# Kernel optimization log

Measured on AMD Instinct MI355X. Metric: run time of the kernel, lower is better.

## Reference

```python
import jax, jax.numpy as jnp
import numpy as np

L, N, H, SQ = 24, 16384, 128, 32
D_OP, D_ATTR, D_FILT, D_OUT = 16, 56, 74, 32
D_IN = 2 * SQ + D_OP + D_ATTR  # 136
EPS = 1e-5
SLOPE = 0.01  # LeakyReLU default


def setup_inputs() -> dict:
    key = jax.random.key(0)
    ks = jax.random.split(key, 24)
    f32 = jnp.float32
    inp = {
        'op_pad': jax.random.normal(ks[0], (L, N, D_OP), f32),
        'attr_pad': jax.random.normal(ks[1], (L, N, D_ATTR), f32),
        'filter_pad': jax.random.normal(ks[2], (L, N, D_FILT), f32),
        'output_pad': jax.random.normal(ks[3], (L, N, D_OUT), f32),
        'mapping_pad': jax.random.randint(ks[4], (L, N, 2), 0, N + 1, jnp.int32),
        'batch_size': 4096,
        # filter / output squeeze linears
        'Wf': jax.random.normal(ks[5], (SQ, D_FILT), f32) * 0.05,
        'bf': jax.random.normal(ks[6], (SQ,), f32) * 0.05,
        'Wo': jax.random.normal(ks[7], (SQ, D_OUT), f32) * 0.05,
        'bo': jax.random.normal(ks[8], (SQ,), f32) * 0.05,
        # batchnorm affine params
        'g1': jnp.ones((SQ,), f32), 'beta1': jnp.zeros((SQ,), f32),
        'g2': jnp.ones((SQ,), f32), 'beta2': jnp.zeros((SQ,), f32),
        # LSTM (PyTorch layout: gates i,f,g,o stacked)
        'Wih': jax.random.normal(ks[9], (4 * H, D_IN), f32) * 0.05,
        'Whh': jax.random.normal(ks[10], (4 * H, H), f32) * 0.05,
        'bih': jax.random.normal(ks[11], (4 * H,), f32) * 0.05,
        'bhh': jax.random.normal(ks[12], (4 * H,), f32) * 0.05,
        # final MLP head
        'W1': jax.random.normal(ks[13], (20, H), f32) * 0.05,
        'b1': jax.random.normal(ks[14], (20,), f32) * 0.05,
        'W2': jax.random.normal(ks[15], (1, 20), f32) * 0.05,
        'b2': jax.random.normal(ks[16], (1,), f32) * 0.05,
    }
    return inp


def _leaky(x):
    return jnp.where(x > 0, x, SLOPE * x)


def _bn(x, g, b):
    # BatchNorm1d in training mode: batch stats (biased var), eps=1e-5
    m = jnp.mean(x, axis=0)
    v = jnp.var(x, axis=0)
    return (x - m) * jax.lax.rsqrt(v + EPS) * g + b


def _forward(op_pad, attr_pad, filter_pad, output_pad, mapping_pad, batch_size,
             Wf, bf, Wo, bo, g1, beta1, g2, beta2, Wih, Whh, bih, bhh, W1, b1, W2, b2):
    l, n = op_pad.shape[0], op_pad.shape[1]
    # squeeze filter / output features, flattened over (L*N)
    fd = _bn(_leaky(filter_pad.reshape(l * n, -1) @ Wf.T + bf), g1, beta1).reshape(l, n, SQ)
    od = _bn(_leaky(output_pad.reshape(l * n, -1) @ Wo.T + bo), g2, beta2).reshape(l, n, SQ)
    lstm_in = jnp.concatenate([op_pad, attr_pad, fd, od], axis=2)  # [L,N,D_IN]

    def step(carry, xs):
        h, c = carry                       # [N,H] previous level states
        x, mapping = xs                    # [N,D_IN], [N,2]
        mask = (mapping != 0)[..., None]   # [N,2,1]
        idx = jnp.maximum(mapping - 1, 0)  # [N,2] gather indices
        gh = jnp.sum(jnp.where(mask, h[idx], 0.0), axis=1) * 0.5  # [N,H]
        gc = jnp.sum(jnp.where(mask, c[idx], 0.0), axis=1) * 0.5
        gates = x @ Wih.T + bih + gh @ Whh.T + bhh  # [N,4H]
        i, f, g, o = jnp.split(gates, 4, axis=1)
        c_new = jax.nn.sigmoid(f) * gc + jax.nn.sigmoid(i) * jnp.tanh(g)
        h_new = jax.nn.sigmoid(o) * jnp.tanh(c_new)
        return (h_new, c_new), None

    z = jnp.zeros((n, H), lstm_in.dtype)
    # loop goes from the deepest level (index L-1) up to 0
    (h, _), _ = jax.lax.scan(step, (z, z), (lstm_in[::-1], mapping_pad[::-1]))
    out = h[:batch_size]
    out = jax.nn.sigmoid((out @ W1.T + b1) @ W2.T + b2)  # [B,1]
    return out


def reference(op_pad, attr_pad, filter_pad, output_pad, mapping_pad, batch_size,
              Wf, bf, Wo, bo, g1, beta1, g2, beta2, Wih, Whh, bih, bhh, W1, b1, W2, b2):
    return _forward(op_pad, attr_pad, filter_pad, output_pad, mapping_pad, batch_size,
                    Wf, bf, Wo, bo, g1, beta1, g2, beta2, Wih, Whh, bih, bhh, W1, b1, W2, b2)
```

## Files before the change

### kernel.cpp

```cpp
#include <hip/hip_runtime.h>
#include <hip/hip_bf16.h>

#define LL 24
#define NN 16384
#define HH 128
#define KP 288
#define LN (LL*NN)

typedef __bf16 bf16;
typedef __attribute__((ext_vector_type(8))) __bf16 bf16x8;
typedef __attribute__((ext_vector_type(2))) __bf16 bf16x2;
typedef __attribute__((ext_vector_type(4))) float f32x4;

__device__ __forceinline__ float sigm(float x){ return 1.f/(1.f+__expf(-x)); }
__device__ __forceinline__ float tanhfast(float x){
    float e = __expf(-2.f*fabsf(x));
    float t = (1.f-e)/(1.f+e);
    return x >= 0.f ? t : -t;
}
__device__ __forceinline__ void gld16(const void* g, void* l){
    __builtin_amdgcn_global_load_lds(
        (const __attribute__((address_space(1))) void*)g,
        (__attribute__((address_space(3))) void*)l, 16, 0, 0);
}

template<int D>
__global__ __launch_bounds__(256) void act_kernel(
    const float* __restrict__ X, const float* __restrict__ W,
    const float* __restrict__ bias, bf16* __restrict__ act,
    float* __restrict__ sums)
{
    __shared__ float w_lds[D*32];
    __shared__ float xs[128*D];
    const int tid = threadIdx.x;
    for (int i = tid; i < D*32; i += 256) {
        int k = i >> 5, ch = i & 31;
        w_lds[i] = W[ch*D + k];
    }
    const int c2 = tid & 15;
    const int rg = tid >> 4;
    const int ch0 = 2*c2, ch1 = ch0+1;
    const float b0 = bias[ch0], b1 = bias[ch1];
    float s0=0.f,s1=0.f,q0=0.f,q1=0.f;
    for (int tile = blockIdx.x; tile < LN/128; tile += gridDim.x) {
        const long row0 = (long)tile*128;
        __syncthreads();
        for (int i = tid; i < 128*D; i += 256) xs[i] = X[row0*D + i];
        __syncthreads();
        float a0[8], a1[8];
        #pragma unroll
        for (int i=0;i<8;++i){ a0[i]=b0; a1[i]=b1; }
        for (int k=0;k<D;++k){
            float w0 = w_lds[(k<<5)+ch0];
            float w1 = w_lds[(k<<5)+ch1];
            #pragma unroll
            for (int i=0;i<8;++i){
                float x = xs[(rg*8+i)*D + k];
                a0[i] = fmaf(x,w0,a0[i]);
                a1[i] = fmaf(x,w1,a1[i]);
            }
        }
        #pragma unroll
        for (int i=0;i<8;++i){
            float v0 = a0[i]; v0 = v0>0.f ? v0 : 0.01f*v0;
            float v1 = a1[i]; v1 = v1>0.f ? v1 : 0.01f*v1;
            bf16x2 pk; pk[0]=(bf16)v0; pk[1]=(bf16)v1;
            *(bf16x2*)&act[(row0 + rg*8+i)*32 + ch0] = pk;
            s0+=v0; q0+=v0*v0; s1+=v1; q1+=v1*v1;
        }
    }
    __syncthreads();
    float* red = xs;
    red[tid]=s0; red[256+tid]=q0; red[512+tid]=s1; red[768+tid]=q1;
    __syncthreads();
    if (tid < 16) {
        float ts0=0,tq0=0,ts1=0,tq1=0;
        for (int r=0;r<16;++r){
            int t = (r<<4) | tid;
            ts0+=red[t]; tq0+=red[256+t]; ts1+=red[512+t]; tq1+=red[768+t];
        }
        atomicAdd(&sums[2*tid],      ts0);
        atomicAdd(&sums[2*tid+1],    ts1);
        atomicAdd(&sums[32+2*tid],   tq0);
        atomicAdd(&sums[32+2*tid+1], tq1);
    }
}

__global__ void prep_wtb(const float* __restrict__ Wih, const float* __restrict__ Whh,
                         const float* __restrict__ bih, const float* __restrict__ bhh,
                         bf16* __restrict__ Wtb, float* __restrict__ b4p)
{
    const int np = blockIdx.x;
    const int k  = threadIdx.x;
    const int gate = (np>>4)&3;
    const int j = gate*128 + (np>>6)*16 + (np&15);
    if (k < KP) {
        float v = 0.f;
        if (k < 136)      v = Wih[(long)j*136 + k];
        else if (k >= 160) v = Whh[(long)j*128 + (k-160)];
        Wtb[(long)np*KP + k] = (bf16)v;
    }
    if (k == 0) b4p[np] = bih[j] + bhh[j];
}

__global__ void prep_stats(const float* __restrict__ stats,
    const float* __restrict__ g1, const float* __restrict__ beta1,
    const float* __restrict__ g2, const float* __restrict__ beta2,
    const float* __restrict__ W1, const float* __restrict__ b1,
    const float* __restrict__ W2, const float* __restrict__ b2,
    float* __restrict__ ss, float* __restrict__ wvb)
{
    const int t = threadIdx.x;
    const float inv = 1.f/(float)LN;
    if (t < 32) {
        float mean = stats[t]*inv;
        float var  = stats[32+t]*inv - mean*mean;
        float sc = g1[t]/sqrtf(var + 1e-5f);
        ss[t] = sc; ss[32+t] = beta1[t] - mean*sc;
    } else if (t < 64) {
        int c = t - 32;
        float mean = stats[64+c]*inv;
        float var  = stats[96+c]*inv - mean*mean;
        float sc = g2[c]/sqrtf(var + 1e-5f);
        ss[64+c] = sc; ss[96+c] = beta2[c] - mean*sc;
    }
    float s = 0.f;
    for (int a=0;a<20;++a) s += W2[a]*W1[a*HH + t];
    wvb[t] = s;
    if (t == 0) {
        float sb = 0.f;
        for (int a=0;a<20;++a) sb += W2[a]*b1[a];
        wvb[128] = sb + b2[0];
    }
}

__global__ __launch_bounds__(256) void build_a(
    const float* __restrict__ op, const float* __restrict__ attr,
    const bf16* __restrict__ actf, const bf16* __restrict__ acto,
    const int* __restrict__ map, const float* __restrict__ ss,
    const bf16* __restrict__ h_prev, bf16* __restrict__ A,
    int l, int first)
{
    const int n0 = blockIdx.x * 32;
    const long lbase = (long)l * NN;
    for (int i = threadIdx.x; i < 32*36; i += 256) {
        const int r = i / 36, c = i - r*36;
        const long n = n0 + r;
        const long e = lbase + n;
        const int k0 = c*8;
        bf16x8 out;
        if (c < 9) {
            const float* src = (c < 2) ? (op + e*16 + k0) : (attr + e*56 + (k0-16));
            float4 f0 = *(const float4*)src;
            float4 f1 = *(const float4*)(src+4);
            out[0]=(bf16)f0.x; out[1]=(bf16)f0.y; out[2]=(bf16)f0.z; out[3]=(bf16)f0.w;
            out[4]=(bf16)f1.x; out[5]=(bf16)f1.y; out[6]=(bf16)f1.z; out[7]=(bf16)f1.w;
        } else if (c < 17) {
            const int ch = (c < 13) ? (k0-72) : (k0-104);
            const bf16* src = (c < 13) ? (actf + e*32 + ch) : (acto + e*32 + ch);
            const float* s = ss + ((c < 13) ? 0 : 64);
            bf16x8 v = *(const bf16x8*)src;
            #pragma unroll
            for (int j=0;j<8;++j)
                out[j] = (bf16)fmaf((float)v[j], s[ch+j], s[32+ch+j]);
        } else if (c < 20) {
            #pragma unroll
            for (int j=0;j<8;++j) out[j] = (bf16)0.f;
        } else {
            const int jj = k0 - 160;
            float g[8] = {0,0,0,0,0,0,0,0};
            if (!first) {
                int2 mp = *(const int2*)&map[e*2];
                if (mp.x) { bf16x8 v = *(const bf16x8*)&h_prev[(long)(mp.x-1)*HH + jj];
                    #pragma unroll
                    for (int j=0;j<8;++j) g[j] += (float)v[j]; }
                if (mp.y) { bf16x8 v = *(const bf16x8*)&h_prev[(long)(mp.y-1)*HH + jj];
                    #pragma unroll
                    for (int j=0;j<8;++j) g[j] += (float)v[j]; }
            }
            #pragma unroll
            for (int j=0;j<8;++j) out[j] = (bf16)(0.5f*g[j]);
        }
        *(bf16x8*)&A[n*KP + k0] = out;
    }
}

__global__ __launch_bounds__(256) void lstm_gemm(
    const bf16* __restrict__ A, const bf16* __restrict__ Wtb,
    const float* __restrict__ b4p, const int* __restrict__ map,
    const float* __restrict__ c_prev, float* __restrict__ c_next,
    bf16* __restrict__ h_next, int l, int first)
{
    __shared__ bf16 As[128*32];
    __shared__ bf16 Bs[128*32];
    const int tid  = threadIdx.x;
    const int bm   = blockIdx.x;
    const int bn   = blockIdx.y;
    const int m0   = bm*128, n0p = bn*128;
    const int lane = tid & 63, w = tid >> 6;
    const int wr   = w >> 1,  wc = w & 1;

    f32x4 acc[4][4];
    #pragma unroll
    for (int ni=0; ni<4; ++ni){
        float b = b4p[n0p + wc*64 + ni*16 + (lane&15)];
        #pragma unroll
        for (int mi=0; mi<4; ++mi) acc[mi][ni] = (f32x4){b,b,b,b};
    }

    const bf16* Ab = A   + (size_t)m0*KP;
    const bf16* Bb = Wtb + (size_t)n0p*KP;
    const int lrr = lane >> 2;
    const int qs  = lane & 3;

    for (int kk=0; kk<9; ++kk){
        __syncthreads();
        #pragma unroll
        for (int hh=0; hh<2; ++hh){
            const int lr = w*32 + hh*16 + lrr;
            const int q  = qs ^ ((lr>>1)&3);
            const size_t go = (size_t)lr*KP + kk*32 + q*8;
            gld16(Ab + go, &As[(w*32 + hh*16)*32]);
            gld16(Bb + go, &Bs[(w*32 + hh*16)*32]);
        }
        __syncthreads();
        bf16x8 af[4], bfr[4];
        #pragma unroll
        for (int t4=0; t4<4; ++t4){
            const int am = wr*64 + t4*16 + (lane&15);
            af[t4] = *(const bf16x8*)&As[am*32 + (((lane>>4) ^ ((am>>1)&3))<<3)];
            const int bn_ = wc*64 + t4*16 + (lane&15);
            bfr[t4] = *(const bf16x8*)&Bs[bn_*32 + (((lane>>4) ^ ((bn_>>1)&3))<<3)];
        }
        #pragma unroll
        for (int mi=0; mi<4; ++mi)
            #pragma unroll
            for (int ni=0; ni<4; ++ni)
                acc[mi][ni] = __builtin_amdgcn_mfma_f32_16x16x32_bf16(
                    af[mi], bfr[ni], acc[mi][ni], 0, 0, 0);
    }

    const long lbase = (long)l * NN;
    const int cell = bn*32 + wc*16 + (lane&15);
    #pragma unroll
    for (int mi=0; mi<4; ++mi){
        const int rbase = m0 + wr*64 + mi*16 + (lane>>4)*4;
        #pragma unroll
        for (int reg=0; reg<4; ++reg){
            const int n = rbase + reg;
            float gc = 0.f;
            if (!first){
                int2 mp = *(const int2*)&map[(lbase+n)*2];
                if (mp.x) gc += c_prev[(long)(mp.x-1)*HH + cell];
                if (mp.y) gc += c_prev[(long)(mp.y-1)*HH + cell];
                gc *= 0.5f;
            }
            float cn = sigm(acc[mi][1][reg])*gc
                     + sigm(acc[mi][0][reg])*tanhfast(acc[mi][2][reg]);
            float hn = sigm(acc[mi][3][reg])*tanhfast(cn);
            c_next[(long)n*HH + cell] = cn;
            h_next[(long)n*HH + cell] = (bf16)hn;
        }
    }
}

__global__ __launch_bounds__(256) void final_k(
    const bf16* __restrict__ h, const float* __restrict__ wvb,
    float* __restrict__ out, int rows)
{
    int gt = blockIdx.x*256 + threadIdx.x;
    int row = gt >> 6;
    int lane = gt & 63;
    if (row >= rows) return;
    float v = fmaf((float)h[(long)row*HH + lane], wvb[lane],
                   (float)h[(long)row*HH + 64 + lane] * wvb[64+lane]);
    #pragma unroll
    for (int off=32; off>0; off>>=1) v += __shfl_down(v, off);
    if (lane == 0) out[row] = sigm(v + wvb[128]);
}

extern "C" void kernel_launch(void* const* d_in, const int* in_sizes, int n_in,
                              void* d_out, int out_size, void* d_ws, size_t ws_size,
                              hipStream_t stream)
{
    const float* op      = (const float*)d_in[0];
    const float* attr    = (const float*)d_in[1];
    const float* filt    = (const float*)d_in[2];
    const float* outp    = (const float*)d_in[3];
    const int*   mapping = (const int*)d_in[4];
    const float* Wf  = (const float*)d_in[6];
    const float* bf_ = (const float*)d_in[7];
    const float* Wo  = (const float*)d_in[8];
    const float* bo  = (const float*)d_in[9];
    const float* g1  = (const float*)d_in[10];
    const float* be1 = (const float*)d_in[11];
    const float* g2  = (const float*)d_in[12];
    const float* be2 = (const float*)d_in[13];
    const float* Wih = (const float*)d_in[14];
    const float* Whh = (const float*)d_in[15];
    const float* bih = (const float*)d_in[16];
    const float* bhh = (const float*)d_in[17];
    const float* W1  = (const float*)d_in[18];
    const float* b1  = (const float*)d_in[19];
    const float* W2  = (const float*)d_in[20];
    const float* b2  = (const float*)d_in[21];

    char* p = (char*)d_ws;
    auto alloc = [&](size_t bytes){ char* r = p; p += (bytes + 255) & ~255ull; return r; };
    bf16* actf = (bf16*)alloc((size_t)LN*32*2);
    bf16* acto = (bf16*)alloc((size_t)LN*32*2);
    bf16* h0   = (bf16*)alloc((size_t)NN*HH*2);
    bf16* h1   = (bf16*)alloc((size_t)NN*HH*2);
    float* c0  = (float*)alloc((size_t)NN*HH*4);
    float* c1  = (float*)alloc((size_t)NN*HH*4);
    bf16* Abuf = (bf16*)alloc((size_t)NN*KP*2);
    bf16* Wtb  = (bf16*)alloc((size_t)512*KP*2);
    float* b4p = (float*)alloc(512*4);
    float* stats=(float*)alloc(128*4);
    float* ssb = (float*)alloc(128*4);
    float* wvb = (float*)alloc(132*4);

    hipMemsetAsync(stats, 0, 128*sizeof(float), stream);
    act_kernel<74><<<768, 256, 0, stream>>>(filt, Wf, bf_, actf, stats);
    act_kernel<32><<<768, 256, 0, stream>>>(outp, Wo, bo, acto, stats+64);
    prep_wtb<<<512, 320, 0, stream>>>(Wih, Whh, bih, bhh, Wtb, b4p);
    prep_stats<<<1, 128, 0, stream>>>(stats, g1, be1, g2, be2, W1, b1, W2, b2, ssb, wvb);

    bf16*  hb[2] = {h0, h1};
    float* cb[2] = {c0, c1};
    for (int t = 0; t < LL; ++t) {
        const int l = (LL-1) - t;
        const int first = (t == 0);
        build_a<<<NN/32, 256, 0, stream>>>(op, attr, actf, acto, mapping, ssb,
                                           hb[t&1], Abuf, l, first);
        lstm_gemm<<<dim3(128,4), 256, 0, stream>>>(Abuf, Wtb, b4p, mapping,
            cb[t&1], cb[(t+1)&1], hb[(t+1)&1], l, first);
    }
    final_k<<<(out_size*64 + 255)/256, 256, 0, stream>>>(hb[0], wvb, (float*)d_out, out_size);
}
```

Measured before the change: 1.346 ms.

## Fuse LSTM input assembly into GEMM and restructure squeeze-linear kernel

The separate build_a kernel is merged into the per-step LSTM GEMM. Each block now assembles its 128-row A tile directly into padded LDS and keeps the full B slice in registers, which removes the global A buffer round trip and one launch per timestep. The trade-off is redundant work: each of the 4 column blocks rebuilds the same A rows, including the h gathers, and the register pressure is high (bq is 36 vectors). The squeeze-linear kernel is also rewritten so that one thread computes all 32 channels per row from bf16-staged inputs, with weights read from global memory and wave shuffles for the batch-norm sums. Staging inputs as bf16 adds rounding before the linear layer.

```diff
diff --git a/kernel.cpp b/kernel.cpp
--- a/kernel.cpp
+++ b/kernel.cpp
@@ -5,6 +5,7 @@
 #define NN 16384
 #define HH 128
 #define KP 288
+#define KPAD 296
 #define LN (LL*NN)
 
 typedef __bf16 bf16;
@@ -18,71 +19,87 @@
     float t = (1.f-e)/(1.f+e);
     return x >= 0.f ? t : -t;
 }
-__device__ __forceinline__ void gld16(const void* g, void* l){
-    __builtin_amdgcn_global_load_lds(
-        (const __attribute__((address_space(1))) void*)g,
-        (__attribute__((address_space(3))) void*)l, 16, 0, 0);
-}
-
-template<int D>
-__global__ __launch_bounds__(256) void act_kernel(
-    const float* __restrict__ X, const float* __restrict__ W,
+
+__global__ void prep_wk(const float* __restrict__ Wf, const float* __restrict__ Wo,
+                        float* __restrict__ Wkf, float* __restrict__ Wko)
+{
+    int t = blockIdx.x*64 + threadIdx.x;
+    if (t < 74*32) {
+        int k = t >> 5, ch = t & 31;
+        Wkf[t] = Wf[ch*74 + k];
+    } else if (t < 74*32 + 32*32) {
+        int t2 = t - 74*32;
+        int k = t2 >> 5, ch = t2 & 31;
+        Wko[t2] = Wo[ch*32 + k];
+    }
+}
+
+template<int D, int XP>
+__global__ __launch_bounds__(256) void act_v3(
+    const float* __restrict__ X, const float* __restrict__ Wk,
     const float* __restrict__ bias, bf16* __restrict__ act,
     float* __restrict__ sums)
 {
-    __shared__ float w_lds[D*32];
-    __shared__ float xs[128*D];
-    const int tid = threadIdx.x;
-    for (int i = tid; i < D*32; i += 256) {
-        int k = i >> 5, ch = i & 31;
-        w_lds[i] = W[ch*D + k];
-    }
-    const int c2 = tid & 15;
-    const int rg = tid >> 4;
-    const int ch0 = 2*c2, ch1 = ch0+1;
-    const float b0 = bias[ch0], b1 = bias[ch1];
-    float s0=0.f,s1=0.f,q0=0.f,q1=0.f;
-    for (int tile = blockIdx.x; tile < LN/128; tile += gridDim.x) {
-        const long row0 = (long)tile*128;
+    __shared__ bf16 xs[256*XP];
+    const int tid  = threadIdx.x;
+    const int lane = tid & 63;
+    float s[32], q[32];
+    #pragma unroll
+    for (int ch=0; ch<32; ++ch){ s[ch]=0.f; q[ch]=0.f; }
+
+    for (int g = blockIdx.x; g < LN/256; g += gridDim.x){
+        const long row0 = (long)g*256;
         __syncthreads();
-        for (int i = tid; i < 128*D; i += 256) xs[i] = X[row0*D + i];
+        for (int i = tid; i < 256*(D/2); i += 256){
+            const int r = i/(D/2), j2 = i - r*(D/2);
+            float2 v = *(const float2*)&X[(row0+r)*D + 2*j2];
+            bf16x2 pk; pk[0]=(bf16)v.x; pk[1]=(bf16)v.y;
+            *(bf16x2*)&xs[r*XP + 2*j2] = pk;
+        }
         __syncthreads();
-        float a0[8], a1[8];
-        #pragma unroll
-        for (int i=0;i<8;++i){ a0[i]=b0; a1[i]=b1; }
-        for (int k=0;k<D;++k){
-            float w0 = w_lds[(k<<5)+ch0];
-            float w1 = w_lds[(k<<5)+ch1];
-            #pragma unroll
-            for (int i=0;i<8;++i){
-                float x = xs[(rg*8+i)*D + k];
-                a0[i] = fmaf(x,w0,a0[i]);
-                a1[i] = fmaf(x,w1,a1[i]);
+
+        float acc[32];
+        #pragma unroll
+        for (int ch=0; ch<32; ++ch) acc[ch] = bias[ch];
+        #pragma unroll 2
+        for (int k2=0; k2<D/2; ++k2){
+            bf16x2 xv = *(const bf16x2*)&xs[tid*XP + 2*k2];
+            const float x0 = (float)xv[0], x1 = (float)xv[1];
+            const float* w0 = Wk + (2*k2)*32;
+            const float* w1 = w0 + 32;
+            #pragma unroll
+            for (int ch=0; ch<32; ++ch){
+                acc[ch] = fmaf(x0, w0[ch], acc[ch]);
+                acc[ch] = fmaf(x1, w1[ch], acc[ch]);
             }
         }
         #pragma unroll
-        for (int i=0;i<8;++i){
-            float v0 = a0[i]; v0 = v0>0.f ? v0 : 0.01f*v0;
-            float v1 = a1[i]; v1 = v1>0.f ? v1 : 0.01f*v1;
-            bf16x2 pk; pk[0]=(bf16)v0; pk[1]=(bf16)v1;
-            *(bf16x2*)&act[(row0 + rg*8+i)*32 + ch0] = pk;
-            s0+=v0; q0+=v0*v0; s1+=v1; q1+=v1*v1;
-        }
-    }
-    __syncthreads();
-    float* red = xs;
-    red[tid]=s0; red[256+tid]=q0; red[512+tid]=s1; red[768+tid]=q1;
-    __syncthreads();
-    if (tid < 16) {
-        float ts0=0,tq0=0,ts1=0,tq1=0;
-        for (int r=0;r<16;++r){
-            int t = (r<<4) | tid;
-            ts0+=red[t]; tq0+=red[256+t]; ts1+=red[512+t]; tq1+=red[768+t];
-        }
-        atomicAdd(&sums[2*tid],      ts0);
-        atomicAdd(&sums[2*tid+1],    ts1);
-        atomicAdd(&sums[32+2*tid],   tq0);
-        atomicAdd(&sums[32+2*tid+1], tq1);
+        for (int gch=0; gch<4; ++gch){
+            bf16x8 pk;
+            #pragma unroll
+            for (int j=0; j<8; ++j){
+                const int ch = gch*8+j;
+                float v = acc[ch]; v = v>0.f ? v : 0.01f*v;
+                pk[j] = (bf16)v;
+                s[ch] += v; q[ch] += v*v;
+            }
+            *(bf16x8*)&act[(row0+tid)*32 + gch*8] = pk;
+        }
+    }
+
+    #pragma unroll
+    for (int ch=0; ch<32; ++ch){
+        float v = s[ch], u = q[ch];
+        #pragma unroll
+        for (int off=32; off>0; off>>=1){
+            v += __shfl_xor(v, off, 64);
+            u += __shfl_xor(u, off, 64);
+        }
+        s[ch]=v; q[ch]=u;
+    }
+    if (lane < 32){
+        atomicAdd(&sums[lane],    s[lane]);
+        atomicAdd(&sums[32+lane], q[lane]);
     }
 }
 
@@ -134,19 +151,27 @@
     }
 }
 
-__global__ __launch_bounds__(256) void build_a(
+__global__ __launch_bounds__(256, 2) void lstm_fused(
     const float* __restrict__ op, const float* __restrict__ attr,
     const bf16* __restrict__ actf, const bf16* __restrict__ acto,
     const int* __restrict__ map, const float* __restrict__ ss,
-    const bf16* __restrict__ h_prev, bf16* __restrict__ A,
+    const bf16* __restrict__ Wtb, const float* __restrict__ b4p,
+    const bf16* __restrict__ h_prev, const float* __restrict__ c_prev,
+    bf16* __restrict__ h_next, float* __restrict__ c_next,
     int l, int first)
 {
-    const int n0 = blockIdx.x * 32;
+    __shared__ bf16 As[128*KPAD];
+    const int tid  = threadIdx.x;
+    const int bm   = blockIdx.x;
+    const int bn   = blockIdx.y;
+    const int m0   = bm*128, n0p = bn*128;
+    const int lane = tid & 63, w = tid >> 6;
+    const int wr   = w >> 1,  wc = w & 1;
     const long lbase = (long)l * NN;
-    for (int i = threadIdx.x; i < 32*36; i += 256) {
+
+    for (int i = tid; i < 128*36; i += 256) {
         const int r = i / 36, c = i - r*36;
-        const long n = n0 + r;
-        const long e = lbase + n;
+        const long e = lbase + m0 + r;
         const int k0 = c*8;
         bf16x8 out;
         if (c < 9) {
@@ -158,11 +183,11 @@
         } else if (c < 17) {
             const int ch = (c < 13) ? (k0-72) : (k0-104);
             const bf16* src = (c < 13) ? (actf + e*32 + ch) : (acto + e*32 + ch);
-            const float* s = ss + ((c < 13) ? 0 : 64);
+            const float* sp = ss + ((c < 13) ? 0 : 64);
             bf16x8 v = *(const bf16x8*)src;
             #pragma unroll
             for (int j=0;j<8;++j)
-                out[j] = (bf16)fmaf((float)v[j], s[ch+j], s[32+ch+j]);
+                out[j] = (bf16)fmaf((float)v[j], sp[ch+j], sp[32+ch+j]);
         } else if (c < 20) {
             #pragma unroll
             for (int j=0;j<8;++j) out[j] = (bf16)0.f;
@@ -181,24 +206,20 @@
             #pragma unroll
             for (int j=0;j<8;++j) out[j] = (bf16)(0.5f*g[j]);
         }
-        *(bf16x8*)&A[n*KP + k0] = out;
-    }
-}
-
-__global__ __launch_bounds__(256) void lstm_gemm(
-    const bf16* __restrict__ A, const bf16* __restrict__ Wtb,
-    const float* __restrict__ b4p, const int* __restrict__ map,
-    const float* __restrict__ c_prev, float* __restrict__ c_next,
-    bf16* __restrict__ h_next, int l, int first)
-{
-    __shared__ bf16 As[128*32];
-    __shared__ bf16 Bs[128*32];
-    const int tid  = threadIdx.x;
-    const int bm   = blockIdx.x;
-    const int bn   = blockIdx.y;
-    const int m0   = bm*128, n0p = bn*128;
-    const int lane = tid & 63, w = tid >> 6;
-    const int wr   = w >> 1,  wc = w & 1;
+        *(bf16x8*)&As[r*KPAD + k0] = out;
+    }
+
+    bf16x8 bq[9][4];
+    {
+        const bf16* Bb = Wtb + (size_t)n0p*KP;
+        const int nb  = wc*64 + (lane&15);
+        const int kof = (lane>>4)*8;
+        #pragma unroll
+        for (int kk=0; kk<9; ++kk)
+            #pragma unroll
+            for (int t4=0; t4<4; ++t4)
+                bq[kk][t4] = *(const bf16x8*)&Bb[(size_t)(nb + t4*16)*KP + kk*32 + kof];
+    }
 
     f32x4 acc[4][4];
     #pragma unroll
@@ -208,39 +229,23 @@
         for (int mi=0; mi<4; ++mi) acc[mi][ni] = (f32x4){b,b,b,b};
     }
 
-    const bf16* Ab = A   + (size_t)m0*KP;
-    const bf16* Bb = Wtb + (size_t)n0p*KP;
-    const int lrr = lane >> 2;
-    const int qs  = lane & 3;
-
+    __syncthreads();
+
+    #pragma unroll
     for (int kk=0; kk<9; ++kk){
-        __syncthreads();
-        #pragma unroll
-        for (int hh=0; hh<2; ++hh){
-            const int lr = w*32 + hh*16 + lrr;
-            const int q  = qs ^ ((lr>>1)&3);
-            const size_t go = (size_t)lr*KP + kk*32 + q*8;
-            gld16(Ab + go, &As[(w*32 + hh*16)*32]);
-            gld16(Bb + go, &Bs[(w*32 + hh*16)*32]);
-        }
-        __syncthreads();
-        bf16x8 af[4], bfr[4];
-        #pragma unroll
-        for (int t4=0; t4<4; ++t4){
-            const int am = wr*64 + t4*16 + (lane&15);
-            af[t4] = *(const bf16x8*)&As[am*32 + (((lane>>4) ^ ((am>>1)&3))<<3)];
-            const int bn_ = wc*64 + t4*16 + (lane&15);
-            bfr[t4] = *(const bf16x8*)&Bs[bn_*32 + (((lane>>4) ^ ((bn_>>1)&3))<<3)];
-        }
+        bf16x8 af[4];
+        #pragma unroll
+        for (int mi=0; mi<4; ++mi)
+            af[mi] = *(const bf16x8*)&As[(wr*64 + mi*16 + (lane&15))*KPAD
+                                         + kk*32 + (lane>>4)*8];
         #pragma unroll
         for (int mi=0; mi<4; ++mi)
             #pragma unroll
             for (int ni=0; ni<4; ++ni)
                 acc[mi][ni] = __builtin_amdgcn_mfma_f32_16x16x32_bf16(
-                    af[mi], bfr[ni], acc[mi][ni], 0, 0, 0);
-    }
-
-    const long lbase = (long)l * NN;
+                    af[mi], bq[kk][ni], acc[mi][ni], 0, 0, 0);
+    }
+
     const int cell = bn*32 + wc*16 + (lane&15);
     #pragma unroll
     for (int mi=0; mi<4; ++mi){
@@ -313,28 +318,27 @@
     bf16* h1   = (bf16*)alloc((size_t)NN*HH*2);
     float* c0  = (float*)alloc((size_t)NN*HH*4);
     float* c1  = (float*)alloc((size_t)NN*HH*4);
-    bf16* Abuf = (bf16*)alloc((size_t)NN*KP*2);
     bf16* Wtb  = (bf16*)alloc((size_t)512*KP*2);
+    float* Wkf = (float*)alloc(74*32*4);
+    float* Wko = (float*)alloc(32*32*4);
     float* b4p = (float*)alloc(512*4);
     float* stats=(float*)alloc(128*4);
     float* ssb = (float*)alloc(128*4);
     float* wvb = (float*)alloc(132*4);
 
+    prep_wk<<<53, 64, 0, stream>>>(Wf, Wo, Wkf, Wko);
+    prep_wtb<<<512, 320, 0, stream>>>(Wih, Whh, bih, bhh, Wtb, b4p);
     hipMemsetAsync(stats, 0, 128*sizeof(float), stream);
-    act_kernel<74><<<768, 256, 0, stream>>>(filt, Wf, bf_, actf, stats);
-    act_kernel<32><<<768, 256, 0, stream>>>(outp, Wo, bo, acto, stats+64);
-    prep_wtb<<<512, 320, 0, stream>>>(Wih, Whh, bih, bhh, Wtb, b4p);
+    act_v3<74,76><<<768, 256, 0, stream>>>(filt, Wkf, bf_, actf, stats);
+    act_v3<32,34><<<768, 256, 0, stream>>>(outp, Wko, bo, acto, stats+64);
     prep_stats<<<1, 128, 0, stream>>>(stats, g1, be1, g2, be2, W1, b1, W2, b2, ssb, wvb);
 
     bf16*  hb[2] = {h0, h1};
     float* cb[2] = {c0, c1};
     for (int t = 0; t < LL; ++t) {
         const int l = (LL-1) - t;
-        const int first = (t == 0);
-        build_a<<<NN/32, 256, 0, stream>>>(op, attr, actf, acto, mapping, ssb,
-                                           hb[t&1], Abuf, l, first);
-        lstm_gemm<<<dim3(128,4), 256, 0, stream>>>(Abuf, Wtb, b4p, mapping,
-            cb[t&1], cb[(t+1)&1], hb[(t+1)&1], l, first);
+        lstm_fused<<<dim3(128,4), 256, 0, stream>>>(op, attr, actf, acto, mapping, ssb,
+            Wtb, b4p, hb[t&1], cb[t&1], hb[(t+1)&1], cb[(t+1)&1], l, t==0);
     }
     final_k<<<(out_size*64 + 255)/256, 256, 0, stream>>>(hb[0], wvb, (float*)d_out, out_size);
 }
```

New measurement: 1.892 ms. +40.5%, slower.
